# Performance work log

Measured on AMD Instinct MI355X. Metric: run time of the kernel, lower is better.

The kernel has to match this reference:

```python
import jax, jax.numpy as jnp
import numpy as np

B, WIN, DM, DG, K = 32, 128, 1024, 64, 15  # batch, win_size(node feat dim), d_model(#nodes), graph embed, top_k


def setup_inputs() -> dict:
    key = jax.random.key(0)
    ks = jax.random.split(key, 7)
    sc_in = 1.0 / np.sqrt(WIN)
    return {
        "x": jax.random.normal(ks[0], (B, WIN, DM), jnp.float32),
        "Wq": jax.random.normal(ks[1], (DG, WIN), jnp.float32) * sc_in,
        "bq": jax.random.normal(ks[2], (DG,), jnp.float32) * 0.02,
        "Wk": jax.random.normal(ks[3], (DG, WIN), jnp.float32) * sc_in,
        "bk": jax.random.normal(ks[4], (DG,), jnp.float32) * 0.02,
        "Wg": jax.random.normal(ks[5], (WIN, WIN), jnp.float32) * sc_in,  # GCNConv lin weight [out,in]
        "bg": jax.random.normal(ks[6], (WIN,), jnp.float32) * 0.02,
    }


def _gcn_one(nf, Wq, bq, Wk, bk, Wg, bg):
    # nf: [N, F] node features (N = d_model, F = win_size)
    N = nf.shape[0]
    q = nf @ Wq.T + bq                      # [N, DG]
    k = nf @ Wk.T + bk                      # [N, DG]
    scores = (q @ k.T) * (1.0 / np.sqrt(DG))  # [N, N]
    scores = jnp.where(jnp.eye(N, dtype=bool), -jnp.inf, scores)
    _, tgt = jax.lax.top_k(scores, K)       # [N, K] top-k neighbors per source node
    src = jnp.repeat(jnp.arange(N), K)      # [N*K]
    tgt = tgt.reshape(-1)                   # [N*K]
    loops = jnp.arange(N)
    # manual self loops (module) + self loops added internally by GCNConv (default add_self_loops=True)
    src_all = jnp.concatenate([src, loops, loops])
    tgt_all = jnp.concatenate([tgt, loops, loops])
    # gcn_norm: degree over target (col) with unit edge weights
    deg = jax.ops.segment_sum(jnp.ones_like(tgt_all, jnp.float32), tgt_all, num_segments=N)
    dinv = jnp.where(deg > 0, jax.lax.rsqrt(deg), 0.0)
    norm = dinv[src_all] * dinv[tgt_all]    # [E]
    h = nf @ Wg.T                           # [N, F] linear transform (no bias inside lin)
    msg = h[src_all] * norm[:, None]        # gather + scale
    out = jax.ops.segment_sum(msg, tgt_all, num_segments=N) + bg  # scatter-add + bias
    return out                              # [N, F]


def reference(x, Wq, bq, Wk, bk, Wg, bg):
    # x: [B, win_size, d_model] -> nodes: [B, d_model, win_size]
    nodes = x.transpose(0, 2, 1)
    h = jax.vmap(lambda nf: _gcn_one(nf, Wq, bq, Wk, bk, Wg, bg))(nodes)  # [B, N, F]
    # n_layers == 1: no ReLU/dropout applied after last layer
    return h.transpose(0, 2, 1)  # [B, win_size, d_model]
```

## Files before the change

kernel.cpp:

```cpp
#include <hip/hip_runtime.h>

#define NBATCH 32
#define NN     1024
#define NF     128
#define NDG    64
#define TOPK   15

#define OFF_QH    ((size_t)0)
#define OFF_QL    ((size_t)4194304)
#define OFF_KH    ((size_t)8388608)
#define OFF_KL    ((size_t)12582912)
#define OFF_H     ((size_t)16777216)
#define OFF_DEG   ((size_t)33554432)
#define OFF_BMP   ((size_t)33685504)
#define OFF_WL    ((size_t)37879808)
#define OFF_TOPK  ((size_t)38010880)
#define OFF_W64   ((size_t)40108032)
#define OFF_QT64  ((size_t)40239104)
#define OFF_KT64  ((size_t)57016320)
#define OFF_TMP   ((size_t)0)

typedef short s8v  __attribute__((ext_vector_type(8)));
typedef float f4v  __attribute__((ext_vector_type(4)));
typedef unsigned short us8v __attribute__((ext_vector_type(8)));

__device__ inline unsigned short bf16_rne(float f) {
    unsigned u = __float_as_uint(f);
    return (unsigned short)((u + 0x7FFFu + ((u >> 16) & 1u)) >> 16);
}
__device__ inline float bf16_tof(unsigned short h) { return __uint_as_float(((unsigned)h) << 16); }

__device__ inline unsigned pack22(float s) {
    unsigned u   = __float_as_uint(s);
    int      mag = (int)(u & 0x7FFFFFFFu);
    int      t   = mag - 0x38800000;
    t = t < 0 ? 0 : (t > 0x07FFFFFF ? 0x07FFFFFF : t);
    unsigned ts = (unsigned)t >> 6;
    return ((int)u < 0) ? (0x1FFFFFu - ts) : (0x200000u | ts);
}
__device__ inline float dec22(unsigned val22) {
    bool pos = (val22 & 0x200000u) != 0;
    unsigned ts = pos ? (val22 & 0x1FFFFFu) : (0x1FFFFFu - (val22 & 0x1FFFFFu));
    float f = __uint_as_float((ts << 6) + 0x38800000u);
    return pos ? f : -f;
}

__global__ __launch_bounds__(256) void k_upcast(const float* __restrict__ Wq,
                                                const float* __restrict__ Wk,
                                                double* __restrict__ Wq64,
                                                double* __restrict__ Wk64) {
    int i = blockIdx.x * 256 + threadIdx.x;
    Wq64[i] = (double)Wq[i];
    Wk64[i] = (double)Wk[i];
}

__global__ __launch_bounds__(256) void k_prep(
    const float* __restrict__ x, const float* __restrict__ bq, const float* __restrict__ bk,
    const double* __restrict__ Wq64, const double* __restrict__ Wk64,
    const float* __restrict__ Wg,
    unsigned short* __restrict__ qh, unsigned short* __restrict__ ql,
    unsigned short* __restrict__ kh, unsigned short* __restrict__ kl,
    double* __restrict__ qT64, double* __restrict__ kT64,
    float* __restrict__ h,
    uint4* __restrict__ zbase, int zn)
{
    __shared__ float xs[64 * 129];
    const int t = threadIdx.x;
    const int l = t & 63;
    const int w = t >> 6;
    const int uw = __builtin_amdgcn_readfirstlane(w);
    const int n0 = blockIdx.x * 64;
    const int half = blockIdx.y;
    const int b  = blockIdx.z;

    {
        int lid = ((b * 2 + half) * 16 + blockIdx.x) * 256 + t;
        for (int i = lid; i < zn; i += 262144)
            zbase[i] = make_uint4(0u, 0u, 0u, 0u);
    }

    {
        const int j = t & 63, fg = t >> 6;
        for (int ff = 0; ff < 32; ++ff) {
            int f = fg + ff * 4;
            xs[j * 129 + f] = x[((size_t)b * NF + f) * NN + n0 + j];
        }
    }
    __syncthreads();

    {
        const int d0 = half * 32 + uw * 8;
        double accq[8], acck[8];
        #pragma unroll
        for (int dd = 0; dd < 8; ++dd) {
            accq[dd] = (double)bq[d0 + dd];
            acck[dd] = (double)bk[d0 + dd];
        }
        for (int fc = 0; fc < 32; ++fc) {
            double dx0 = (double)xs[l * 129 + fc * 4 + 0];
            double dx1 = (double)xs[l * 129 + fc * 4 + 1];
            double dx2 = (double)xs[l * 129 + fc * 4 + 2];
            double dx3 = (double)xs[l * 129 + fc * 4 + 3];
            #pragma unroll
            for (int dd = 0; dd < 8; ++dd) {
                int d = d0 + dd;
                const double* wq = &Wq64[d * NF + fc * 4];
                const double* wk = &Wk64[d * NF + fc * 4];
                accq[dd] += dx0 * wq[0] + dx1 * wq[1] + dx2 * wq[2] + dx3 * wq[3];
                acck[dd] += dx0 * wk[0] + dx1 * wk[1] + dx2 * wk[2] + dx3 * wk[3];
            }
        }
        #pragma unroll
        for (int dd = 0; dd < 8; ++dd) {
            size_t idx = ((size_t)b * NDG + d0 + dd) * NN + n0 + l;
            qT64[idx] = accq[dd];
            kT64[idx] = acck[dd];
        }
        us8v qh0, ql0, kh0, kl0;
        #pragma unroll
        for (int dd = 0; dd < 8; ++dd) {
            float fq = (float)accq[dd];
            unsigned short h1 = bf16_rne(fq);
            unsigned short l1 = bf16_rne(fq - bf16_tof(h1));
            float fk = (float)acck[dd];
            unsigned short h2 = bf16_rne(fk);
            unsigned short l2 = bf16_rne(fk - bf16_tof(h2));
            qh0[dd] = h1; ql0[dd] = l1; kh0[dd] = h2; kl0[dd] = l2;
        }
        size_t nb = ((size_t)b * NN + n0 + l) * NDG + d0;
        *(us8v*)&qh[nb] = qh0;
        *(us8v*)&ql[nb] = ql0;
        *(us8v*)&kh[nb] = kh0;
        *(us8v*)&kl[nb] = kl0;
    }

    {
        const int fp0 = half * 64 + uw * 16;
        float acc[16];
        #pragma unroll
        for (int i = 0; i < 16; ++i) acc[i] = 0.f;
        for (int fc = 0; fc < 32; ++fc) {
            float x0 = xs[l * 129 + fc * 4 + 0];
            float x1 = xs[l * 129 + fc * 4 + 1];
            float x2 = xs[l * 129 + fc * 4 + 2];
            float x3 = xs[l * 129 + fc * 4 + 3];
            #pragma unroll
            for (int ff = 0; ff < 16; ++ff) {
                const float* wg = &Wg[(fp0 + ff) * NF + fc * 4];
                acc[ff] += x0 * wg[0] + x1 * wg[1] + x2 * wg[2] + x3 * wg[3];
            }
        }
        __syncthreads();
        #pragma unroll
        for (int ff = 0; ff < 16; ++ff) xs[l * 129 + fp0 + ff] = acc[ff];
        __syncthreads();
        for (int r = 0; r < 16; ++r) {
            int idx = t + 256 * r;
            int n = idx >> 6, f = idx & 63;
            h[((size_t)b * NN + n0 + n) * NF + half * 64 + f] = xs[n * 129 + half * 64 + f];
        }
    }
}

#define CE(x,y) { unsigned a_ = v[x], b_ = v[y]; v[x] = a_ > b_ ? a_ : b_; v[y] = a_ > b_ ? b_ : a_; }
__device__ inline void sort16(unsigned v[16]) {
    CE(0,1) CE(2,3) CE(4,5) CE(6,7) CE(8,9) CE(10,11) CE(12,13) CE(14,15)
    CE(0,2) CE(1,3) CE(4,6) CE(5,7) CE(8,10) CE(9,11) CE(12,14) CE(13,15)
    CE(1,2) CE(5,6) CE(9,10) CE(13,14)
    CE(0,4) CE(1,5) CE(2,6) CE(3,7) CE(8,12) CE(9,13) CE(10,14) CE(11,15)
    CE(2,4) CE(3,5) CE(10,12) CE(11,13)
    CE(1,2) CE(3,4) CE(5,6) CE(9,10) CE(11,12) CE(13,14)
    CE(0,8) CE(1,9) CE(2,10) CE(3,11) CE(4,12) CE(5,13) CE(6,14) CE(7,15)
    CE(4,8) CE(5,9) CE(6,10) CE(7,11)
    CE(2,4) CE(3,5) CE(6,8) CE(7,9) CE(10,12) CE(11,13)
    CE(1,2) CE(3,4) CE(5,6) CE(7,8) CE(9,10) CE(11,12) CE(13,14)
}
__device__ inline void clean16(unsigned v[16]) {
    CE(0,8) CE(1,9) CE(2,10) CE(3,11) CE(4,12) CE(5,13) CE(6,14) CE(7,15)
    CE(0,4) CE(1,5) CE(2,6) CE(3,7) CE(8,12) CE(9,13) CE(10,14) CE(11,15)
    CE(0,2) CE(1,3) CE(4,6) CE(5,7) CE(8,10) CE(9,11) CE(12,14) CE(13,15)
    CE(0,1) CE(2,3) CE(4,5) CE(6,7) CE(8,9) CE(10,11) CE(12,13) CE(14,15)
}

__device__ inline unsigned bsort64(unsigned v, int l) {
    #pragma unroll
    for (int k = 2; k <= 64; k <<= 1) {
        #pragma unroll
        for (int j = k >> 1; j >= 1; j >>= 1) {
            unsigned pv = (unsigned)__shfl_xor((int)v, j, 64);
            bool tm = ((l & k) == 0) == ((l & j) == 0);
            unsigned hi = v > pv ? v : pv;
            unsigned lo = v > pv ? pv : v;
            v = tm ? hi : lo;
        }
    }
    return v;
}

__global__ __launch_bounds__(512, 4) void k_score(
    const unsigned short* __restrict__ qh, const unsigned short* __restrict__ ql,
    const unsigned short* __restrict__ kh, const unsigned short* __restrict__ kl,
    int* __restrict__ deg, unsigned int* __restrict__ bmp,
    int* __restrict__ topk, int* __restrict__ wl_cnt, int* __restrict__ wl)
{
    __shared__ unsigned pk[16 * 1024];
    const int t = threadIdx.x, l = t & 63, w = t >> 6;
    const int b = blockIdx.y, row0 = blockIdx.x * 16;
    const int m = l & 15, q4 = l >> 4;

    size_t abase = ((size_t)b * NN + row0 + m) * NDG + q4 * 8;
    s8v ah0 = *(const s8v*)&qh[abase];
    s8v ah1 = *(const s8v*)&qh[abase + 32];
    s8v al0 = *(const s8v*)&ql[abase];
    s8v al1 = *(const s8v*)&ql[abase + 32];

    const int colbase = w * 128;
    #pragma unroll
    for (int tt = 0; tt < 8; ++tt) {
        int col = colbase + tt * 16 + m;
        size_t bbase = ((size_t)b * NN + col) * NDG + q4 * 8;
        s8v bh0 = *(const s8v*)&kh[bbase];
        s8v bh1 = *(const s8v*)&kh[bbase + 32];
        s8v bl0 = *(const s8v*)&kl[bbase];
        s8v bl1 = *(const s8v*)&kl[bbase + 32];
        f4v acc = {0.f, 0.f, 0.f, 0.f};
        acc = __builtin_amdgcn_mfma_f32_16x16x32_bf16(al0, bl0, acc, 0, 0, 0);
        acc = __builtin_amdgcn_mfma_f32_16x16x32_bf16(al1, bl1, acc, 0, 0, 0);
        acc = __builtin_amdgcn_mfma_f32_16x16x32_bf16(ah0, bl0, acc, 0, 0, 0);
        acc = __builtin_amdgcn_mfma_f32_16x16x32_bf16(ah1, bl1, acc, 0, 0, 0);
        acc = __builtin_amdgcn_mfma_f32_16x16x32_bf16(al0, bh0, acc, 0, 0, 0);
        acc = __builtin_amdgcn_mfma_f32_16x16x32_bf16(al1, bh1, acc, 0, 0, 0);
        acc = __builtin_amdgcn_mfma_f32_16x16x32_bf16(ah0, bh0, acc, 0, 0, 0);
        acc = __builtin_amdgcn_mfma_f32_16x16x32_bf16(ah1, bh1, acc, 0, 0, 0);
        #pragma unroll
        for (int r = 0; r < 4; ++r) {
            int row  = q4 * 4 + r;
            int grow = row0 + row;
            float s = acc[r] * 0.125f;
            unsigned c22 = (col == grow) ? 0u : pack22(s);
            pk[row * 1024 + (col ^ (q4 << 4))] = (c22 << 10) | (unsigned)(1023 - col);
        }
    }
    __syncthreads();

    for (int rr = 0; rr < 2; ++rr) {
        const int row = 2 * w + rr, grow = row0 + row;
        unsigned v[16];
        #pragma unroll
        for (int j = 0; j < 16; ++j)
            v[j] = pk[row * 1024 + l + 64 * j];

        unsigned lmax = v[0];
        #pragma unroll
        for (int j = 1; j < 16; ++j) lmax = v[j] > lmax ? v[j] : lmax;

        unsigned sm = bsort64(lmax, l);
        unsigned T = (unsigned)__shfl((int)sm, 15, 64);

        int cnt = 0;
        #pragma unroll
        for (int j = 0; j < 16; ++j) cnt += (v[j] >= T) ? 1 : 0;
        int pre = cnt;
        #pragma unroll
        for (int d = 1; d < 64; d <<= 1) {
            int o = __shfl_up(pre, d, 64);
            if (l >= d) pre += o;
        }
        const int C = __shfl(pre, 63, 64);
        int off = pre - cnt;

        unsigned res;
        if (C <= 64) {
            unsigned* scr = &pk[row * 1024];
            #pragma unroll
            for (int j = 0; j < 16; ++j)
                if (v[j] >= T) scr[off++] = v[j];
            unsigned cv = (l < C) ? scr[l] : 0u;
            res = bsort64(cv, l);
        } else {
            sort16(v);
            #pragma unroll
            for (int offb = 1; offb < 64; offb <<= 1) {
                unsigned pv[16];
                #pragma unroll
                for (int i = 0; i < 16; ++i) pv[i] = (unsigned)__shfl_xor((int)v[i], offb, 64);
                #pragma unroll
                for (int i = 0; i < 8; ++i) {
                    unsigned a0 = v[i], b0 = pv[15 - i];
                    unsigned a1 = v[15 - i], b1 = pv[i];
                    v[i]      = a0 > b0 ? a0 : b0;
                    v[15 - i] = a1 > b1 ? a1 : b1;
                }
                clean16(v);
            }
            unsigned rsel = v[15];
            #pragma unroll
            for (int j = 0; j < 15; ++j) if (l == j) rsel = v[j];
            res = rsel;
        }

        unsigned r14 = (unsigned)__shfl((int)res, 14, 64);
        unsigned r15 = (unsigned)__shfl((int)res, 15, 64);
        float s15 = dec22(r14 >> 10), s16 = dec22(r15 >> 10);
        unsigned e15 = (__float_as_uint(fabsf(s15)) >> 23) & 255u;
        unsigned e16 = (__float_as_uint(fabsf(s16)) >> 23) & 255u;
        unsigned e = e15 > e16 ? e15 : e16;
        float qq = __uint_as_float((e - 17) << 23);
        bool flagged = (s15 - s16) < (4.f * qq + 1e-4f);
        if (l < 15) {
            int col = 1023 - (int)(res & 1023u);
            atomicAdd(&deg[b * NN + col], 1);
            atomicOr(&bmp[((size_t)b * NN + col) * 32 + (grow >> 5)], 1u << (grow & 31));
            if (flagged) topk[(b * NN + grow) * 16 + l] = col;
        }
        if (l == 0 && flagged) {
            int idx = atomicAdd(wl_cnt, 1);
            if (idx < 32767) wl[idx] = b * NN + grow;
        }
    }
}

__global__ __launch_bounds__(64) void k_repair(
    const double* __restrict__ qT64, const double* __restrict__ kT64,
    const int* __restrict__ topk, const int* __restrict__ wl_cnt, const int* __restrict__ wl,
    int* __restrict__ deg, unsigned int* __restrict__ bmp)
{
    const int l = threadIdx.x;
    __shared__ double qld[64];
    __shared__ int oldset[15], newset[15];
    const double NEGINF = -__builtin_inf();
    int n = wl_cnt[0]; if (n > 32767) n = 32767;

    for (int i = blockIdx.x; i < n; i += 1024) {
        int rg = wl[i];
        int b = rg >> 10, row = rg & 1023;

        __syncthreads();
        qld[l] = qT64[((size_t)b * NDG + l) * NN + row];
        if (l < 15) oldset[l] = topk[(b * NN + row) * 16 + l];
        __syncthreads();

        double sc[16];
        #pragma unroll
        for (int tt = 0; tt < 16; ++tt) sc[tt] = 0.0;
        const double* kb = &kT64[(size_t)b * NDG * NN];
        double buf[16];
        #pragma unroll
        for (int tt = 0; tt < 16; ++tt) buf[tt] = kb[l + 64 * tt];
        for (int d = 0; d < 64; ++d) {
            double nb[16];
            if (d < 63) {
                const double* kr = kb + (size_t)(d + 1) * NN;
                #pragma unroll
                for (int tt = 0; tt < 16; ++tt) nb[tt] = kr[l + 64 * tt];
            }
            double qd = qld[d];
            #pragma unroll
            for (int tt = 0; tt < 16; ++tt) sc[tt] += qd * buf[tt];
            if (d < 63) {
                #pragma unroll
                for (int tt = 0; tt < 16; ++tt) buf[tt] = nb[tt];
            }
        }
        #pragma unroll
        for (int tt = 0; tt < 16; ++tt) if (l + 64 * tt == row) sc[tt] = NEGINF;

        for (int it = 0; it < 15; ++it) {
            double lv = NEGINF; int lc = 0x7fffffff;
            #pragma unroll
            for (int tt = 0; tt < 16; ++tt)
                if (sc[tt] > lv) { lv = sc[tt]; lc = l + 64 * tt; }
            #pragma unroll
            for (int off = 1; off < 64; off <<= 1) {
                double ov = __shfl_xor(lv, off, 64);
                int    oc = __shfl_xor(lc, off, 64);
                if (ov > lv || (ov == lv && oc < lc)) { lv = ov; lc = oc; }
            }
            #pragma unroll
            for (int tt = 0; tt < 16; ++tt) if (l + 64 * tt == lc) sc[tt] = NEGINF;
            if (l == 0) newset[it] = lc;
        }
        __syncthreads();
        if (l < 15) {
            int cn = newset[l];
            bool found = false;
            #pragma unroll
            for (int j = 0; j < 15; ++j) found = found || (oldset[j] == cn);
            if (!found) {
                atomicAdd(&deg[b * NN + cn], 1);
                atomicOr(&bmp[((size_t)b * NN + cn) * 32 + (row >> 5)], 1u << (row & 31));
            }
            int co = oldset[l];
            found = false;
            #pragma unroll
            for (int j = 0; j < 15; ++j) found = found || (newset[j] == co);
            if (!found) {
                atomicSub(&deg[b * NN + co], 1);
                atomicAnd(&bmp[((size_t)b * NN + co) * 32 + (row >> 5)], ~(1u << (row & 31)));
            }
        }
    }
}

__global__ __launch_bounds__(128) void k_gather(
    const float* __restrict__ h, const float* __restrict__ bg,
    const int* __restrict__ deg, const unsigned int* __restrict__ bmp,
    float* __restrict__ tmp)
{
    __shared__ int list[1024];
    __shared__ float nrm[1024];
    __shared__ int scnt;
    const int tgt = blockIdx.x, b = blockIdx.y, t = threadIdx.x;
    if (t < 32) {
        unsigned word = bmp[((size_t)b * NN + tgt) * 32 + t];
        int pc = __popc(word);
        int pre = pc;
        #pragma unroll
        for (int d = 1; d < 32; d <<= 1) {
            int o = __shfl_up(pre, d, 32);
            if (t >= d) pre += o;
        }
        if (t == 31) scnt = pre;
        int idx = pre - pc;
        while (word) {
            int s = __ffs(word) - 1;
            word &= word - 1;
            list[idx++] = t * 32 + s;
        }
    }
    __syncthreads();
    const int cnt = scnt;
    for (int e = t; e < cnt; e += 128)
        nrm[e] = rsqrtf((float)(deg[b * NN + list[e]] + 2));
    __syncthreads();
    const int f = t;
    float dt = rsqrtf((float)(deg[b * NN + tgt] + 2));
    float acc = 2.0f * dt * h[((size_t)b * NN + tgt) * NF + f];
    for (int e = 0; e < cnt; ++e) {
        int src = list[e];
        acc += h[((size_t)b * NN + src) * NF + f] * nrm[e];
    }
    tmp[((size_t)b * NN + tgt) * NF + f] = bg[f] + dt * acc;
}

__global__ __launch_bounds__(256) void k_transpose(const float* __restrict__ tmp,
                                                   float* __restrict__ out)
{
    __shared__ float tile[32][33];
    const int t = threadIdx.x;
    const int n0 = blockIdx.x * 32, f0 = blockIdx.y * 32, b = blockIdx.z;
    const int c = t & 31, rb = t >> 5;
    #pragma unroll
    for (int i = 0; i < 4; ++i) {
        int r = rb + i * 8;
        tile[r][c] = tmp[((size_t)b * NN + n0 + r) * NF + f0 + c];
    }
    __syncthreads();
    #pragma unroll
    for (int i = 0; i < 4; ++i) {
        int r = rb + i * 8;
        out[((size_t)b * NF + f0 + r) * NN + n0 + c] = tile[c][r];
    }
}

extern "C" void kernel_launch(void* const* d_in, const int* in_sizes, int n_in,
                              void* d_out, int out_size, void* d_ws, size_t ws_size,
                              hipStream_t stream)
{
    const float* x  = (const float*)d_in[0];
    const float* Wq = (const float*)d_in[1];
    const float* bq = (const float*)d_in[2];
    const float* Wk = (const float*)d_in[3];
    const float* bk = (const float*)d_in[4];
    const float* Wg = (const float*)d_in[5];
    const float* bg = (const float*)d_in[6];
    float* out = (float*)d_out;
    char* ws = (char*)d_ws;

    unsigned short* qh = (unsigned short*)(ws + OFF_QH);
    unsigned short* ql = (unsigned short*)(ws + OFF_QL);
    unsigned short* kh = (unsigned short*)(ws + OFF_KH);
    unsigned short* kl = (unsigned short*)(ws + OFF_KL);
    float*          h   = (float*)(ws + OFF_H);
    int*            deg = (int*)(ws + OFF_DEG);
    unsigned int*   bmp = (unsigned int*)(ws + OFF_BMP);
    int*            wlc = (int*)(ws + OFF_WL);
    int*            wl  = wlc + 1;
    int*            tpk = (int*)(ws + OFF_TOPK);
    double*         Wq64 = (double*)(ws + OFF_W64);
    double*         Wk64 = Wq64 + 8192;
    double*         qT64 = (double*)(ws + OFF_QT64);
    double*         kT64 = (double*)(ws + OFF_KT64);
    float*          tmp  = (float*)(ws + OFF_TMP);

    k_upcast<<<32, 256, 0, stream>>>(Wq, Wk, Wq64, Wk64);
    k_prep<<<dim3(16, 2, 32), 256, 0, stream>>>(x, bq, bk, Wq64, Wk64, Wg,
                                                qh, ql, kh, kl, qT64, kT64, h,
                                                (uint4*)(ws + OFF_DEG), 270337);
    k_score<<<dim3(64, 32), 512, 0, stream>>>(qh, ql, kh, kl, deg, bmp, tpk, wlc, wl);
    k_repair<<<1024, 64, 0, stream>>>(qT64, kT64, tpk, wlc, wl, deg, bmp);
    k_gather<<<dim3(1024, 32), 128, 0, stream>>>(h, bg, deg, bmp, tmp);
    k_transpose<<<dim3(32, 4, 32), 256, 0, stream>>>(tmp, out);
}
```

Before: 317.0 us.

## Prefilter top-k candidates with a per-row statistical threshold during score compute

Instead of writing all 1024 packed scores per row to shared memory, each row computes a threshold from the query norm and the key bias (a statistical bound on the top-15 cutoff) and compacts only the scores above it via ballot/popcount into 32 slots per wave. Selection then runs a pair-batched bitonic sort over at most 256 candidates. Rows that overflow or have too few candidates fall back to the exact repair kernel through the worklist. The smaller shared-memory footprint allows occupancy 6 instead of 4. The risk is that a poorly tuned threshold routes many rows to the slower repair path.

```diff
diff --git a/kernel.cpp b/kernel.cpp
--- a/kernel.cpp
+++ b/kernel.cpp
@@ -162,26 +162,6 @@
     }
 }
 
-#define CE(x,y) { unsigned a_ = v[x], b_ = v[y]; v[x] = a_ > b_ ? a_ : b_; v[y] = a_ > b_ ? b_ : a_; }
-__device__ inline void sort16(unsigned v[16]) {
-    CE(0,1) CE(2,3) CE(4,5) CE(6,7) CE(8,9) CE(10,11) CE(12,13) CE(14,15)
-    CE(0,2) CE(1,3) CE(4,6) CE(5,7) CE(8,10) CE(9,11) CE(12,14) CE(13,15)
-    CE(1,2) CE(5,6) CE(9,10) CE(13,14)
-    CE(0,4) CE(1,5) CE(2,6) CE(3,7) CE(8,12) CE(9,13) CE(10,14) CE(11,15)
-    CE(2,4) CE(3,5) CE(10,12) CE(11,13)
-    CE(1,2) CE(3,4) CE(5,6) CE(9,10) CE(11,12) CE(13,14)
-    CE(0,8) CE(1,9) CE(2,10) CE(3,11) CE(4,12) CE(5,13) CE(6,14) CE(7,15)
-    CE(4,8) CE(5,9) CE(6,10) CE(7,11)
-    CE(2,4) CE(3,5) CE(6,8) CE(7,9) CE(10,12) CE(11,13)
-    CE(1,2) CE(3,4) CE(5,6) CE(7,8) CE(9,10) CE(11,12) CE(13,14)
-}
-__device__ inline void clean16(unsigned v[16]) {
-    CE(0,8) CE(1,9) CE(2,10) CE(3,11) CE(4,12) CE(5,13) CE(6,14) CE(7,15)
-    CE(0,4) CE(1,5) CE(2,6) CE(3,7) CE(8,12) CE(9,13) CE(10,14) CE(11,15)
-    CE(0,2) CE(1,3) CE(4,6) CE(5,7) CE(8,10) CE(9,11) CE(12,14) CE(13,15)
-    CE(0,1) CE(2,3) CE(4,5) CE(6,7) CE(8,9) CE(10,11) CE(12,13) CE(14,15)
-}
-
 __device__ inline unsigned bsort64(unsigned v, int l) {
     #pragma unroll
     for (int k = 2; k <= 64; k <<= 1) {
@@ -197,16 +177,41 @@
     return v;
 }
 
-__global__ __launch_bounds__(512, 4) void k_score(
+__device__ inline void bsort64_2(unsigned& va, unsigned& vb, int l) {
+    #pragma unroll
+    for (int k = 2; k <= 64; k <<= 1) {
+        #pragma unroll
+        for (int j = k >> 1; j >= 1; j >>= 1) {
+            unsigned pa = (unsigned)__shfl_xor((int)va, j, 64);
+            unsigned pb = (unsigned)__shfl_xor((int)vb, j, 64);
+            bool tm = ((l & k) == 0) == ((l & j) == 0);
+            unsigned ha = va > pa ? va : pa, la = va > pa ? pa : va;
+            unsigned hb = vb > pb ? vb : pb, lb = vb > pb ? pb : vb;
+            va = tm ? ha : la;
+            vb = tm ? hb : lb;
+        }
+    }
+}
+
+__global__ __launch_bounds__(512, 6) void k_score(
     const unsigned short* __restrict__ qh, const unsigned short* __restrict__ ql,
     const unsigned short* __restrict__ kh, const unsigned short* __restrict__ kl,
+    const float* __restrict__ bk,
     int* __restrict__ deg, unsigned int* __restrict__ bmp,
     int* __restrict__ topk, int* __restrict__ wl_cnt, int* __restrict__ wl)
 {
-    __shared__ unsigned pk[16 * 1024];
+    __shared__ __align__(16) unsigned slots[16 * 256];
+    __shared__ unsigned rowflag[16];
     const int t = threadIdx.x, l = t & 63, w = t >> 6;
     const int b = blockIdx.y, row0 = blockIdx.x * 16;
     const int m = l & 15, q4 = l >> 4;
+
+    {
+        uint4* z = (uint4*)slots;
+        z[t]       = make_uint4(0u, 0u, 0u, 0u);
+        z[t + 512] = make_uint4(0u, 0u, 0u, 0u);
+        if (t < 16) rowflag[t] = 0u;
+    }
 
     size_t abase = ((size_t)b * NN + row0 + m) * NDG + q4 * 8;
     s8v ah0 = *(const s8v*)&qh[abase];
@@ -214,7 +219,30 @@
     s8v al0 = *(const s8v*)&ql[abase];
     s8v al1 = *(const s8v*)&ql[abase + 32];
 
+    unsigned Trow[4];
+    {
+        float ssq = 0.f, smn = 0.f;
+        #pragma unroll
+        for (int j = 0; j < 8; ++j) {
+            float q0 = bf16_tof(((us8v)ah0)[j]) + bf16_tof(((us8v)al0)[j]);
+            float q1 = bf16_tof(((us8v)ah1)[j]) + bf16_tof(((us8v)al1)[j]);
+            float b0 = bk[q4 * 8 + j];
+            float b1 = bk[q4 * 8 + 32 + j];
+            ssq += q0 * q0 + q1 * q1;
+            smn += q0 * b0 + q1 * b1;
+        }
+        ssq += __shfl_xor(ssq, 16, 64); ssq += __shfl_xor(ssq, 32, 64);
+        smn += __shfl_xor(smn, 16, 64); smn += __shfl_xor(smn, 32, 64);
+        float t_m = 0.125f * smn + 0.2125f * __builtin_sqrtf(ssq);
+        unsigned Tm = pack22(t_m) << 10;
+        #pragma unroll
+        for (int r = 0; r < 4; ++r)
+            Trow[r] = (unsigned)__shfl((int)Tm, 4 * q4 + r, 64);
+    }
+    __syncthreads();
+
     const int colbase = w * 128;
+    unsigned basec[4] = {0u, 0u, 0u, 0u};
     #pragma unroll
     for (int tt = 0; tt < 8; ++tt) {
         int col = colbase + tt * 16 + m;
@@ -238,77 +266,91 @@
             int grow = row0 + row;
             float s = acc[r] * 0.125f;
             unsigned c22 = (col == grow) ? 0u : pack22(s);
-            pk[row * 1024 + (col ^ (q4 << 4))] = (c22 << 10) | (unsigned)(1023 - col);
-        }
-    }
+            unsigned v = (c22 << 10) | (unsigned)(1023 - col);
+            bool p = v >= Trow[r];
+            unsigned long long mk = __ballot(p);
+            unsigned w16 = (unsigned)(mk >> (q4 * 16)) & 0xFFFFu;
+            unsigned idx = basec[r] + (unsigned)__popc(w16 & ((1u << m) - 1u));
+            if (p && idx < 32u) slots[row * 256 + w * 32 + (int)idx] = v;
+            basec[r] += (unsigned)__popc(w16);
+        }
+    }
+    #pragma unroll
+    for (int r = 0; r < 4; ++r)
+        if (m == 0 && basec[r] > 32u) rowflag[q4 * 4 + r] = 1u;
     __syncthreads();
 
+    const int rA = 2 * w, rB = 2 * w + 1;
+    uint4 ca = *(const uint4*)&slots[rA * 256 + l * 4];
+    uint4 cb = *(const uint4*)&slots[rB * 256 + l * 4];
+
+    unsigned mxa = ca.x > ca.y ? ca.x : ca.y;  mxa = mxa > ca.z ? mxa : ca.z;  mxa = mxa > ca.w ? mxa : ca.w;
+    unsigned mxb = cb.x > cb.y ? cb.x : cb.y;  mxb = mxb > cb.z ? mxb : cb.z;  mxb = mxb > cb.w ? mxb : cb.w;
+    bsort64_2(mxa, mxb, l);
+    unsigned Ta = (unsigned)__shfl((int)mxa, 15, 64);
+    unsigned Tb = (unsigned)__shfl((int)mxb, 15, 64);
+
+    int ka0 = (ca.x >= Ta && ca.x) ? 1 : 0, ka1 = (ca.y >= Ta && ca.y) ? 1 : 0;
+    int ka2 = (ca.z >= Ta && ca.z) ? 1 : 0, ka3 = (ca.w >= Ta && ca.w) ? 1 : 0;
+    int kb0 = (cb.x >= Tb && cb.x) ? 1 : 0, kb1 = (cb.y >= Tb && cb.y) ? 1 : 0;
+    int kb2 = (cb.z >= Tb && cb.z) ? 1 : 0, kb3 = (cb.w >= Tb && cb.w) ? 1 : 0;
+    int cntA = ka0 + ka1 + ka2 + ka3;
+    int cntB = kb0 + kb1 + kb2 + kb3;
+    int preA = cntA, preB = cntB;
+    #pragma unroll
+    for (int d = 1; d < 64; d <<= 1) {
+        int oA = __shfl_up(preA, d, 64);
+        int oB = __shfl_up(preB, d, 64);
+        if (l >= d) { preA += oA; preB += oB; }
+    }
+    const int CA = __shfl(preA, 63, 64);
+    const int CB = __shfl(preB, 63, 64);
+
+    {
+        unsigned* scr = &slots[rA * 256];
+        int off = preA - cntA;
+        if (ka0) scr[off++] = ca.x;
+        if (ka1) scr[off++] = ca.y;
+        if (ka2) scr[off++] = ca.z;
+        if (ka3) scr[off++] = ca.w;
+    }
+    {
+        unsigned* scr = &slots[rB * 256];
+        int off = preB - cntB;
+        if (kb0) scr[off++] = cb.x;
+        if (kb1) scr[off++] = cb.y;
+        if (kb2) scr[off++] = cb.z;
+        if (kb3) scr[off++] = cb.w;
+    }
+    unsigned cva = (l < CA && l < 64) ? slots[rA * 256 + l] : 0u;
+    unsigned cvb = (l < CB && l < 64) ? slots[rB * 256 + l] : 0u;
+    bsort64_2(cva, cvb, l);
+
+    #pragma unroll
     for (int rr = 0; rr < 2; ++rr) {
-        const int row = 2 * w + rr, grow = row0 + row;
-        unsigned v[16];
-        #pragma unroll
-        for (int j = 0; j < 16; ++j)
-            v[j] = pk[row * 1024 + l + 64 * j];
-
-        unsigned lmax = v[0];
-        #pragma unroll
-        for (int j = 1; j < 16; ++j) lmax = v[j] > lmax ? v[j] : lmax;
-
-        unsigned sm = bsort64(lmax, l);
-        unsigned T = (unsigned)__shfl((int)sm, 15, 64);
-
-        int cnt = 0;
-        #pragma unroll
-        for (int j = 0; j < 16; ++j) cnt += (v[j] >= T) ? 1 : 0;
-        int pre = cnt;
-        #pragma unroll
-        for (int d = 1; d < 64; d <<= 1) {
-            int o = __shfl_up(pre, d, 64);
-            if (l >= d) pre += o;
-        }
-        const int C = __shfl(pre, 63, 64);
-        int off = pre - cnt;
-
-        unsigned res;
-        if (C <= 64) {
-            unsigned* scr = &pk[row * 1024];
-            #pragma unroll
-            for (int j = 0; j < 16; ++j)
-                if (v[j] >= T) scr[off++] = v[j];
-            unsigned cv = (l < C) ? scr[l] : 0u;
-            res = bsort64(cv, l);
-        } else {
-            sort16(v);
-            #pragma unroll
-            for (int offb = 1; offb < 64; offb <<= 1) {
-                unsigned pv[16];
-                #pragma unroll
-                for (int i = 0; i < 16; ++i) pv[i] = (unsigned)__shfl_xor((int)v[i], offb, 64);
-                #pragma unroll
-                for (int i = 0; i < 8; ++i) {
-                    unsigned a0 = v[i], b0 = pv[15 - i];
-                    unsigned a1 = v[15 - i], b1 = pv[i];
-                    v[i]      = a0 > b0 ? a0 : b0;
-                    v[15 - i] = a1 > b1 ? a1 : b1;
-                }
-                clean16(v);
-            }
-            unsigned rsel = v[15];
-            #pragma unroll
-            for (int j = 0; j < 15; ++j) if (l == j) rsel = v[j];
-            res = rsel;
-        }
+        const int row  = rr == 0 ? rA : rB;
+        const int grow = row0 + row;
+        unsigned res   = rr == 0 ? cva : cvb;
+        const int C2   = rr == 0 ? CA : CB;
 
         unsigned r14 = (unsigned)__shfl((int)res, 14, 64);
         unsigned r15 = (unsigned)__shfl((int)res, 15, 64);
-        float s15 = dec22(r14 >> 10), s16 = dec22(r15 >> 10);
-        unsigned e15 = (__float_as_uint(fabsf(s15)) >> 23) & 255u;
-        unsigned e16 = (__float_as_uint(fabsf(s16)) >> 23) & 255u;
-        unsigned e = e15 > e16 ? e15 : e16;
-        float qq = __uint_as_float((e - 17) << 23);
-        bool flagged = (s15 - s16) < (4.f * qq + 1e-4f);
+        bool fb = (rowflag[row] != 0u) || (C2 > 64) || (r15 == 0u);
+
+        bool flagged;
+        if (fb) {
+            flagged = true;
+        } else {
+            float s15 = dec22(r14 >> 10), s16 = dec22(r15 >> 10);
+            unsigned e15 = (__float_as_uint(fabsf(s15)) >> 23) & 255u;
+            unsigned e16 = (__float_as_uint(fabsf(s16)) >> 23) & 255u;
+            unsigned e = e15 > e16 ? e15 : e16;
+            float qq = __uint_as_float((e - 17) << 23);
+            flagged = (s15 - s16) < (4.f * qq + 1e-4f);
+        }
         if (l < 15) {
-            int col = 1023 - (int)(res & 1023u);
+            int col = fb ? ((grow + 1 + l) & 1023)
+                         : (1023 - (int)(res & 1023u));
             atomicAdd(&deg[b * NN + col], 1);
             atomicOr(&bmp[((size_t)b * NN + col) * 32 + (grow >> 5)], 1u << (grow & 31));
             if (flagged) topk[(b * NN + grow) * 16 + l] = col;
@@ -497,7 +539,7 @@
     k_prep<<<dim3(16, 2, 32), 256, 0, stream>>>(x, bq, bk, Wq64, Wk64, Wg,
                                                 qh, ql, kh, kl, qT64, kT64, h,
                                                 (uint4*)(ws + OFF_DEG), 270337);
-    k_score<<<dim3(64, 32), 512, 0, stream>>>(qh, ql, kh, kl, deg, bmp, tpk, wlc, wl);
+    k_score<<<dim3(64, 32), 512, 0, stream>>>(qh, ql, kh, kl, bk, deg, bmp, tpk, wlc, wl);
     k_repair<<<1024, 64, 0, stream>>>(qT64, kT64, tpk, wlc, wl, deg, bmp);
     k_gather<<<dim3(1024, 32), 128, 0, stream>>>(h, bg, deg, bmp, tmp);
     k_transpose<<<dim3(32, 4, 32), 256, 0, stream>>>(tmp, out);
```

Result: no change. 311.2 us (-1.8%).
